# Kernel optimization log

Hardware: AMD Instinct MI355X
Metric: run time of the kernel (lower is better)

## Reference

```python
import jax, jax.numpy as jnp
import numpy as np

N, E, F, H = 50000, 160000, 512, 32
EPS = 1e-5  # BatchNorm eps


def setup_inputs() -> dict:
    key = jax.random.key(0)
    ks = jax.random.split(key, 16)
    s = lambda fan: 1.0 / np.sqrt(fan)
    inp = {
        "x": jax.random.normal(ks[0], (N, 2), jnp.float32),
        "edge_index": jax.random.randint(ks[1], (2, E), 0, N, jnp.int64),
        "face": jax.random.normal(ks[2], (N, F), jnp.float32),
        # encoder: Linear(2,32) -> BN(32) -> PReLU -> Dropout(0) -> Linear(32,32)
        "W1": jax.random.uniform(ks[3], (2, H), jnp.float32, -s(2), s(2)),
        "b1": jnp.zeros((H,), jnp.float32),
        "gamma": jnp.ones((H,), jnp.float32),
        "beta": jnp.zeros((H,), jnp.float32),
        "alpha": jnp.full((1,), 0.25, jnp.float32),  # PReLU default
        "W2": jax.random.uniform(ks[4], (H, H), jnp.float32, -s(H), s(H)),
        "b2": jnp.zeros((H,), jnp.float32),
        "w0": jax.random.uniform(ks[5], (H, 1), jnp.float32, -s(H), s(H)),
        "b0": jnp.zeros((1,), jnp.float32),
        "Wg": jax.random.uniform(ks[6], (H, H), jnp.float32, -s(H), s(H)),
        "bg": jnp.zeros((H,), jnp.float32),
        "wf": jax.random.uniform(ks[7], (H, 1), jnp.float32, -s(H), s(H)),
        "bf": jnp.zeros((1,), jnp.float32),
    }
    return inp


def _encoder(x, W1, b1, gamma, beta, alpha, W2, b2):
    h = x @ W1 + b1
    mu = h.mean(0)
    var = h.var(0)  # biased, matching torch BN training math
    h = (h - mu) * jax.lax.rsqrt(var + EPS) * gamma + beta
    h = jnp.where(h >= 0, h, alpha * h)  # PReLU
    return h @ W2 + b2  # dropout p=0


def _gcn_face(h, edge_index, face, Wg, bg):
    # Face-similarity weighted GCN: w_ij = cos(face_i, face_j),
    # symmetric normalization with self loops (weight 1).
    src, dst = edge_index[0], edge_index[1]
    fn = face * jax.lax.rsqrt(jnp.sum(face * face, axis=1, keepdims=True) + 1e-12)
    ew = jnp.sum(fn[src] * fn[dst], axis=-1)  # [E]
    n = h.shape[0]
    deg = jax.ops.segment_sum(ew, dst, num_segments=n) + 1.0  # + self loop
    norm = ew * jax.lax.rsqrt(deg[src] * deg[dst])  # [E]
    agg = jax.ops.segment_sum(norm[:, None] * h[src], dst, num_segments=n)
    agg = agg + h / deg[:, None]  # self-loop term 1/deg_i
    return agg @ Wg + bg


def reference(x, edge_index, face, W1, b1, gamma, beta, alpha, W2, b2,
              w0, b0, Wg, bg, wf, bf):
    emb = _encoder(x, W1, b1, gamma, beta, alpha, W2, b2)      # [N,32]
    gcn = _gcn_face(emb, edge_index, face, Wg, bg)             # [N,32]
    linear_scores = (emb @ w0 + b0).squeeze(-1)                # [N]
    gcn_scores = (gcn @ wf + bf).squeeze(-1)                   # [N]
    return linear_scores + gcn_scores
```

## Files before the change

### kernel.cpp

```cpp
#include <hip/hip_runtime.h>

#define EPS_BN 1e-5f
#define FDIM 512
#define F4   128
#define HDIM 32
#define NB_XS 64

__device__ __forceinline__ int dot4i8(unsigned a, unsigned b) {
#if __has_builtin(__builtin_amdgcn_sdot4)
    return __builtin_amdgcn_sdot4((int)a, (int)b, 0, false);
#else
    int s;
    s  = (int)(signed char)(a      ) * (int)(signed char)(b      );
    s += (int)(signed char)(a >>  8) * (int)(signed char)(b >>  8);
    s += (int)(signed char)(a >> 16) * (int)(signed char)(b >> 16);
    s += (int)(signed char)(a >> 24) * (int)(signed char)(b >> 24);
    return s;
#endif
}

__global__ __launch_bounds__(256)
void k_prep(const float* __restrict__ face,
            const float* __restrict__ x,
            uint2* __restrict__ qrows,
            float* __restrict__ scales,
            float* __restrict__ deg,
            float* __restrict__ part,
            int n, int qb) {
    __shared__ float red[4][5];
    if ((int)blockIdx.x < qb) {
        int row  = (int)((blockIdx.x * 256 + threadIdx.x) >> 6);
        int lane = threadIdx.x & 63;
        if (row >= n) return;
        const float4* f4 = (const float4*)face + (size_t)row * F4;
        float4 a = f4[lane];
        float4 b = f4[lane + 64];
        float ss = a.x*a.x + a.y*a.y + a.z*a.z + a.w*a.w
                 + b.x*b.x + b.y*b.y + b.z*b.z + b.w*b.w;
        float mx = fmaxf(fmaxf(fmaxf(fabsf(a.x), fabsf(a.y)),
                               fmaxf(fabsf(a.z), fabsf(a.w))),
                         fmaxf(fmaxf(fabsf(b.x), fabsf(b.y)),
                               fmaxf(fabsf(b.z), fabsf(b.w))));
        #pragma unroll
        for (int off = 32; off > 0; off >>= 1) {
            ss += __shfl_xor(ss, off);
            mx  = fmaxf(mx, __shfl_xor(mx, off));
        }
        float rn = rsqrtf(ss + 1e-12f);
        float qs = (mx > 0.f) ? 127.0f / mx : 0.f;
        unsigned da =  ((unsigned)(__float2int_rn(a.x*qs) & 255))
                    | (((unsigned)(__float2int_rn(a.y*qs) & 255)) << 8)
                    | (((unsigned)(__float2int_rn(a.z*qs) & 255)) << 16)
                    | (((unsigned)(__float2int_rn(a.w*qs) & 255)) << 24);
        unsigned db =  ((unsigned)(__float2int_rn(b.x*qs) & 255))
                    | (((unsigned)(__float2int_rn(b.y*qs) & 255)) << 8)
                    | (((unsigned)(__float2int_rn(b.z*qs) & 255)) << 16)
                    | (((unsigned)(__float2int_rn(b.w*qs) & 255)) << 24);
        qrows[(size_t)row * 64 + lane] = make_uint2(da, db);
        if (lane == 0) {
            scales[row] = mx * rn * (1.0f / 127.0f);
            deg[row]    = 0.f;
        }
    } else {
        int bid = (int)blockIdx.x - qb;
        float s0=0.f, s1=0.f, s00=0.f, s01=0.f, s11=0.f;
        for (int i = bid * 256 + threadIdx.x; i < n; i += NB_XS * 256) {
            float2 xv = ((const float2*)x)[i];
            s0  += xv.x;       s1  += xv.y;
            s00 += xv.x*xv.x;  s01 += xv.x*xv.y;  s11 += xv.y*xv.y;
        }
        #pragma unroll
        for (int off = 32; off > 0; off >>= 1) {
            s0  += __shfl_xor(s0,  off);
            s1  += __shfl_xor(s1,  off);
            s00 += __shfl_xor(s00, off);
            s01 += __shfl_xor(s01, off);
            s11 += __shfl_xor(s11, off);
        }
        int lane = threadIdx.x & 63, w = threadIdx.x >> 6;
        if (lane == 0) {
            red[w][0]=s0; red[w][1]=s1; red[w][2]=s00; red[w][3]=s01; red[w][4]=s11;
        }
        __syncthreads();
        if (threadIdx.x < 5) {
            part[bid * 5 + threadIdx.x] =
                red[0][threadIdx.x] + red[1][threadIdx.x]
              + red[2][threadIdx.x] + red[3][threadIdx.x];
        }
    }
}

__global__ void k_params(const float* __restrict__ part,
                         const float* __restrict__ W1,
                         const float* __restrict__ b1,
                         const float* __restrict__ gamma,
                         const float* __restrict__ beta,
                         const float* __restrict__ Wg,
                         const float* __restrict__ bg,
                         const float* __restrict__ wf,
                         const float* __restrict__ b0,
                         const float* __restrict__ bf,
                         float* __restrict__ params, int n) {
    __shared__ float xsl[5];
    int t = threadIdx.x;
    if (t < 5) {
        float s = 0.f;
        for (int i = 0; i < NB_XS; ++i) s += part[i * 5 + t];
        xsl[t] = s;
    }
    __syncthreads();
    float invN = 1.0f / (float)n;
    float m0 = xsl[0]*invN, m1 = xsl[1]*invN;
    float c00 = xsl[2]*invN - m0*m0;
    float c01 = xsl[3]*invN - m0*m1;
    float c11 = xsl[4]*invN - m1*m1;
    if (t < HDIM) {
        float w0j = W1[t], w1j = W1[HDIM + t];
        float mu  = m0*w0j + m1*w1j + b1[t];
        float var = c00*w0j*w0j + 2.f*c01*w0j*w1j + c11*w1j*w1j;
        float a   = gamma[t] * rsqrtf(var + EPS_BN);
        params[t]        = a;
        params[HDIM + t] = beta[t] - mu*a;
        float v = 0.f;
        for (int m = 0; m < HDIM; ++m) v += Wg[t*HDIM + m] * wf[m];
        params[2*HDIM + t] = v;
    } else if (t == HDIM) {
        float c = b0[0] + bf[0];
        for (int m = 0; m < HDIM; ++m) c += bg[m] * wf[m];
        params[3*HDIM] = c;
    }
}

__global__ __launch_bounds__(256)
void k_main(const float* __restrict__ x,
            const float* __restrict__ W1, const float* __restrict__ b1,
            const float* __restrict__ alpha,
            const float* __restrict__ W2, const float* __restrict__ b2,
            const float* __restrict__ w0,
            const float* __restrict__ params,
            const uint4* __restrict__ qrows,
            const float* __restrict__ scales,
            const int* __restrict__ src,
            const int* __restrict__ dst,
            float* __restrict__ ew,
            float* __restrict__ deg,
            float* __restrict__ sarr,
            float* __restrict__ out,
            int n, int ne, int nbn) {
    __shared__ float sW2[HDIM*HDIM];
    __shared__ float sW1[2*HDIM], sb1[HDIM], sa[HDIM], sbsh[HDIM];
    __shared__ float sv[HDIM], sw0[HDIM], sb2[HDIM];
    __shared__ float sc, salpha;

    if ((int)blockIdx.x < nbn) {
        for (int i = threadIdx.x; i < HDIM*HDIM; i += blockDim.x) sW2[i] = W2[i];
        if (threadIdx.x < 2*HDIM) sW1[threadIdx.x] = W1[threadIdx.x];
        if (threadIdx.x < HDIM) {
            sb1[threadIdx.x]  = b1[threadIdx.x];
            sa[threadIdx.x]   = params[threadIdx.x];
            sbsh[threadIdx.x] = params[HDIM + threadIdx.x];
            sv[threadIdx.x]   = params[2*HDIM + threadIdx.x];
            sw0[threadIdx.x]  = w0[threadIdx.x];
            sb2[threadIdx.x]  = b2[threadIdx.x];
        }
        if (threadIdx.x == 0) { sc = params[3*HDIM]; salpha = alpha[0]; }
        __syncthreads();
        int i = blockIdx.x * blockDim.x + threadIdx.x;
        if (i >= n) return;

        float2 xv = ((const float2*)x)[i];
        float h[HDIM];
        #pragma unroll
        for (int j = 0; j < HDIM; ++j) {
            float t = xv.x*sW1[j] + xv.y*sW1[HDIM + j] + sb1[j];
            t = sa[j]*t + sbsh[j];
            h[j] = (t >= 0.f) ? t : salpha*t;
        }
        float em[HDIM];
        #pragma unroll
        for (int k = 0; k < HDIM; ++k) em[k] = sb2[k];
        #pragma unroll
        for (int j = 0; j < HDIM; ++j) {
            float hj = h[j];
            #pragma unroll
            for (int k = 0; k < HDIM; ++k) em[k] += hj * sW2[j*HDIM + k];
        }
        float sdot = 0.f, ldot = 0.f;
        #pragma unroll
        for (int k = 0; k < HDIM; ++k) { sdot += em[k]*sv[k]; ldot += em[k]*sw0[k]; }
        sarr[i] = sdot;
        out[i]  = ldot + sc;
    } else {
        int e  = ((int)blockIdx.x - nbn) * 16 + (int)(threadIdx.x >> 4);
        int gl = threadIdx.x & 15;
        if (e >= ne) return;
        int si = src[e], di = dst[e];
        const uint4* rs = qrows + (size_t)si * 32;
        const uint4* rd = qrows + (size_t)di * 32;
        uint4 a0 = rs[gl], a1 = rs[gl + 16];
        uint4 b0 = rd[gl], b1 = rd[gl + 16];
        int acc = dot4i8(a0.x, b0.x) + dot4i8(a0.y, b0.y)
                + dot4i8(a0.z, b0.z) + dot4i8(a0.w, b0.w)
                + dot4i8(a1.x, b1.x) + dot4i8(a1.y, b1.y)
                + dot4i8(a1.z, b1.z) + dot4i8(a1.w, b1.w);
        #pragma unroll
        for (int off = 8; off > 0; off >>= 1) acc += __shfl_xor(acc, off);
        if (gl == 0) {
            float w = (float)acc * scales[si] * scales[di];
            ew[e] = w;
            atomicAdd(&deg[di], w);
        }
    }
}

__global__ void k_finish(const int* __restrict__ src,
                         const int* __restrict__ dst,
                         const float* __restrict__ ew,
                         const float* __restrict__ deg,
                         const float* __restrict__ sarr,
                         float* __restrict__ out, int ne, int n) {
    int t = blockIdx.x * blockDim.x + threadIdx.x;
    if (t < ne) {
        int si = src[t], di = dst[t];
        float w = ew[t] * rsqrtf((deg[si] + 1.f) * (deg[di] + 1.f)) * sarr[si];
        atomicAdd(&out[di], w);
    } else if (t < ne + n) {
        int i = t - ne;
        atomicAdd(&out[i], sarr[i] / (deg[i] + 1.f));
    }
}

extern "C" void kernel_launch(void* const* d_in, const int* in_sizes, int n_in,
                              void* d_out, int out_size, void* d_ws, size_t ws_size,
                              hipStream_t stream) {
    const float* x     = (const float*)d_in[0];
    const int*   ei    = (const int*)  d_in[1];
    const float* face  = (const float*)d_in[2];
    const float* W1    = (const float*)d_in[3];
    const float* b1    = (const float*)d_in[4];
    const float* gamma = (const float*)d_in[5];
    const float* beta  = (const float*)d_in[6];
    const float* alpha = (const float*)d_in[7];
    const float* W2    = (const float*)d_in[8];
    const float* b2    = (const float*)d_in[9];
    const float* w0    = (const float*)d_in[10];
    const float* b0    = (const float*)d_in[11];
    const float* Wg    = (const float*)d_in[12];
    const float* bg    = (const float*)d_in[13];
    const float* wf    = (const float*)d_in[14];
    const float* bf    = (const float*)d_in[15];

    const int n  = in_sizes[0] / 2;
    const int ne = in_sizes[1] / 2;
    const int* src = ei;
    const int* dst = ei + ne;

    float* ws     = (float*)d_ws;
    uint2* qrows  = (uint2*)ws;
    float* after  = ws + (size_t)n * 128;
    float* deg    = after;
    float* scales = after + n;
    float* sarr   = after + 2*(size_t)n;
    float* ew     = after + 3*(size_t)n;
    float* part   = after + 3*(size_t)n + ne;
    float* params = part + NB_XS*5 + 3;
    float* out    = (float*)d_out;

    const int qb  = (n + 3) / 4;
    const int nbn = (n + 255) / 256;
    const int ebk = (ne + 15) / 16;

    k_prep  <<<qb + NB_XS, 256, 0, stream>>>(face, x, qrows, scales, deg,
                                             part, n, qb);
    k_params<<<1, 64, 0, stream>>>(part, W1, b1, gamma, beta, Wg, bg, wf,
                                   b0, bf, params, n);
    k_main  <<<nbn + ebk, 256, 0, stream>>>(x, W1, b1, alpha, W2, b2, w0,
                                            params, (const uint4*)qrows,
                                            scales, src, dst, ew, deg, sarr,
                                            out, n, ne, nbn);
    k_finish<<<(ne + n + 255) / 256, 256, 0, stream>>>(src, dst, ew, deg,
                                                       sarr, out, ne, n);
}
```

Baseline: 66.46 us.

## Bucket-sort edges by destination and remap edge blocks across XCDs

Builds a destination-bucket histogram and prefix sum, with last-block detection, inside the prep kernel. A scatter pass then reorders edges by dst>>6, so the edge cosine kernel reads destination rows and updates deg with more locality. The k_params launch is folded into prep via an atomic ticket, and edge blocks are remapped so contiguous bucket ranges land on the same XCD. Each edge now uses 8 lanes instead of 16. In exchange it adds a memset, atomic-heavy histogram and scatter passes, and extra workspace traffic.

```diff
diff --git a/kernel.cpp b/kernel.cpp
--- a/kernel.cpp
+++ b/kernel.cpp
@@ -5,6 +5,8 @@
 #define F4   128
 #define HDIM 32
 #define NB_XS 64
+#define NBH   64
+#define MAXBKT 1024
 
 __device__ __forceinline__ int dot4i8(unsigned a, unsigned b) {
 #if __has_builtin(__builtin_amdgcn_sdot4)
@@ -19,18 +21,32 @@
 #endif
 }
 
+__device__ __forceinline__ float atomicReadF(float* p) { return atomicAdd(p, 0.0f); }
+__device__ __forceinline__ int   atomicReadI(int* p)   { return atomicAdd(p, 0); }
+
 __global__ __launch_bounds__(256)
 void k_prep(const float* __restrict__ face,
             const float* __restrict__ x,
+            const int* __restrict__ dst,
             uint2* __restrict__ qrows,
             float* __restrict__ scales,
             float* __restrict__ deg,
-            float* __restrict__ part,
-            int n, int qb) {
-    __shared__ float red[4][5];
+            float* __restrict__ xs,
+            int*   __restrict__ tick,
+            int*   __restrict__ hist,
+            int*   __restrict__ bucket_ptr,
+            const float* __restrict__ W1, const float* __restrict__ b1,
+            const float* __restrict__ gamma, const float* __restrict__ beta,
+            const float* __restrict__ Wg, const float* __restrict__ bg,
+            const float* __restrict__ wf, const float* __restrict__ b0,
+            const float* __restrict__ bf,
+            float* __restrict__ params,
+            int n, int ne, int qb, int nbkt) {
+    int tid = threadIdx.x;
+
     if ((int)blockIdx.x < qb) {
-        int row  = (int)((blockIdx.x * 256 + threadIdx.x) >> 6);
-        int lane = threadIdx.x & 63;
+        int row  = (int)((blockIdx.x * 256 + tid) >> 6);
+        int lane = tid & 63;
         if (row >= n) return;
         const float4* f4 = (const float4*)face + (size_t)row * F4;
         float4 a = f4[lane];
@@ -61,10 +77,15 @@
             scales[row] = mx * rn * (1.0f / 127.0f);
             deg[row]    = 0.f;
         }
-    } else {
+        return;
+    }
+
+    if ((int)blockIdx.x < qb + NB_XS) {
+        __shared__ float red[4][5];
+        __shared__ int amlast;
         int bid = (int)blockIdx.x - qb;
         float s0=0.f, s1=0.f, s00=0.f, s01=0.f, s11=0.f;
-        for (int i = bid * 256 + threadIdx.x; i < n; i += NB_XS * 256) {
+        for (int i = bid * 256 + tid; i < n; i += NB_XS * 256) {
             float2 xv = ((const float2*)x)[i];
             s0  += xv.x;       s1  += xv.y;
             s00 += xv.x*xv.x;  s01 += xv.x*xv.y;  s11 += xv.y*xv.y;
@@ -77,82 +98,98 @@
             s01 += __shfl_xor(s01, off);
             s11 += __shfl_xor(s11, off);
         }
-        int lane = threadIdx.x & 63, w = threadIdx.x >> 6;
+        int lane = tid & 63, w = tid >> 6;
         if (lane == 0) {
             red[w][0]=s0; red[w][1]=s1; red[w][2]=s00; red[w][3]=s01; red[w][4]=s11;
         }
         __syncthreads();
-        if (threadIdx.x < 5) {
-            part[bid * 5 + threadIdx.x] =
-                red[0][threadIdx.x] + red[1][threadIdx.x]
-              + red[2][threadIdx.x] + red[3][threadIdx.x];
-        }
-    }
-}
-
-__global__ void k_params(const float* __restrict__ part,
-                         const float* __restrict__ W1,
-                         const float* __restrict__ b1,
-                         const float* __restrict__ gamma,
-                         const float* __restrict__ beta,
-                         const float* __restrict__ Wg,
-                         const float* __restrict__ bg,
-                         const float* __restrict__ wf,
-                         const float* __restrict__ b0,
-                         const float* __restrict__ bf,
-                         float* __restrict__ params, int n) {
-    __shared__ float xsl[5];
-    int t = threadIdx.x;
-    if (t < 5) {
-        float s = 0.f;
-        for (int i = 0; i < NB_XS; ++i) s += part[i * 5 + t];
-        xsl[t] = s;
-    }
-    __syncthreads();
-    float invN = 1.0f / (float)n;
-    float m0 = xsl[0]*invN, m1 = xsl[1]*invN;
-    float c00 = xsl[2]*invN - m0*m0;
-    float c01 = xsl[3]*invN - m0*m1;
-    float c11 = xsl[4]*invN - m1*m1;
-    if (t < HDIM) {
-        float w0j = W1[t], w1j = W1[HDIM + t];
-        float mu  = m0*w0j + m1*w1j + b1[t];
-        float var = c00*w0j*w0j + 2.f*c01*w0j*w1j + c11*w1j*w1j;
-        float a   = gamma[t] * rsqrtf(var + EPS_BN);
-        params[t]        = a;
-        params[HDIM + t] = beta[t] - mu*a;
-        float v = 0.f;
-        for (int m = 0; m < HDIM; ++m) v += Wg[t*HDIM + m] * wf[m];
-        params[2*HDIM + t] = v;
-    } else if (t == HDIM) {
-        float c = b0[0] + bf[0];
-        for (int m = 0; m < HDIM; ++m) c += bg[m] * wf[m];
-        params[3*HDIM] = c;
+        if (tid < 5) {
+            atomicAdd(&xs[tid], red[0][tid] + red[1][tid] + red[2][tid] + red[3][tid]);
+        }
+        if (tid == 0) {
+            __threadfence();
+            amlast = (atomicAdd(&tick[0], 1) == NB_XS - 1);
+        }
+        __syncthreads();
+        if (!amlast) return;
+        __shared__ float xsl[5];
+        if (tid < 5) xsl[tid] = atomicReadF(&xs[tid]);
+        __syncthreads();
+        float invN = 1.0f / (float)n;
+        float m0 = xsl[0]*invN, m1 = xsl[1]*invN;
+        float c00 = xsl[2]*invN - m0*m0;
+        float c01 = xsl[3]*invN - m0*m1;
+        float c11 = xsl[4]*invN - m1*m1;
+        if (tid < HDIM) {
+            float w0j = W1[tid], w1j = W1[HDIM + tid];
+            float mu  = m0*w0j + m1*w1j + b1[tid];
+            float var = c00*w0j*w0j + 2.f*c01*w0j*w1j + c11*w1j*w1j;
+            float aa  = gamma[tid] * rsqrtf(var + EPS_BN);
+            params[tid]        = aa;
+            params[HDIM + tid] = beta[tid] - mu*aa;
+            float v = 0.f;
+            for (int m = 0; m < HDIM; ++m) v += Wg[tid*HDIM + m] * wf[m];
+            params[2*HDIM + tid] = v;
+        } else if (tid == HDIM) {
+            float c = b0[0] + bf[0];
+            for (int m = 0; m < HDIM; ++m) c += bg[m] * wf[m];
+            params[3*HDIM] = c;
+        }
+        return;
+    }
+
+    {
+        __shared__ int amlast;
+        int bid = (int)blockIdx.x - qb - NB_XS;
+        for (int e = bid * 256 + tid; e < ne; e += NBH * 256)
+            atomicAdd(&hist[dst[e] >> 6], 1);
+        if (tid == 0) {
+            __threadfence();
+            amlast = (atomicAdd(&tick[1], 1) == NBH - 1);
+        }
+        __syncthreads();
+        if (!amlast) return;
+        __shared__ int sh[MAXBKT];
+        __shared__ int tsum[256];
+        for (int k = tid; k < MAXBKT; k += 256)
+            sh[k] = (k < nbkt) ? atomicReadI(&hist[k]) : 0;
+        __syncthreads();
+        int k0 = tid * 4;
+        int a0 = sh[k0], a1 = sh[k0+1], a2 = sh[k0+2], a3 = sh[k0+3];
+        int p0 = a0, p1 = p0 + a1, p2 = p1 + a2, p3 = p2 + a3;
+        tsum[tid] = p3;
+        __syncthreads();
+        for (int off = 1; off < 256; off <<= 1) {
+            int v = (tid >= off) ? tsum[tid - off] : 0;
+            __syncthreads();
+            tsum[tid] += v;
+            __syncthreads();
+        }
+        int base = (tid > 0) ? tsum[tid - 1] : 0;
+        if (k0     < MAXBKT) bucket_ptr[k0]     = base;
+        if (k0 + 1 < MAXBKT) bucket_ptr[k0 + 1] = base + p0;
+        if (k0 + 2 < MAXBKT) bucket_ptr[k0 + 2] = base + p1;
+        if (k0 + 3 < MAXBKT) bucket_ptr[k0 + 3] = base + p2;
     }
 }
 
 __global__ __launch_bounds__(256)
-void k_main(const float* __restrict__ x,
-            const float* __restrict__ W1, const float* __restrict__ b1,
-            const float* __restrict__ alpha,
-            const float* __restrict__ W2, const float* __restrict__ b2,
-            const float* __restrict__ w0,
-            const float* __restrict__ params,
-            const uint4* __restrict__ qrows,
-            const float* __restrict__ scales,
-            const int* __restrict__ src,
-            const int* __restrict__ dst,
-            float* __restrict__ ew,
-            float* __restrict__ deg,
-            float* __restrict__ sarr,
-            float* __restrict__ out,
-            int n, int ne, int nbn) {
-    __shared__ float sW2[HDIM*HDIM];
-    __shared__ float sW1[2*HDIM], sb1[HDIM], sa[HDIM], sbsh[HDIM];
-    __shared__ float sv[HDIM], sw0[HDIM], sb2[HDIM];
-    __shared__ float sc, salpha;
-
+void k_mid(const float* __restrict__ x,
+           const float* __restrict__ W1, const float* __restrict__ b1,
+           const float* __restrict__ alpha,
+           const float* __restrict__ W2, const float* __restrict__ b2,
+           const float* __restrict__ w0,
+           const float* __restrict__ params,
+           const int* __restrict__ src, const int* __restrict__ dst,
+           int* __restrict__ bucket_ptr,
+           int* __restrict__ se_src, int* __restrict__ se_dst,
+           float* __restrict__ sarr, float* __restrict__ out,
+           int n, int ne, int nbn) {
     if ((int)blockIdx.x < nbn) {
+        __shared__ float sW2[HDIM*HDIM];
+        __shared__ float sW1[2*HDIM], sb1[HDIM], sa[HDIM], sbsh[HDIM];
+        __shared__ float sv[HDIM], sw0[HDIM], sb2[HDIM];
+        __shared__ float sc, salpha;
         for (int i = threadIdx.x; i < HDIM*HDIM; i += blockDim.x) sW2[i] = W2[i];
         if (threadIdx.x < 2*HDIM) sW1[threadIdx.x] = W1[threadIdx.x];
         if (threadIdx.x < HDIM) {
@@ -167,7 +204,6 @@
         __syncthreads();
         int i = blockIdx.x * blockDim.x + threadIdx.x;
         if (i >= n) return;
-
         float2 xv = ((const float2*)x)[i];
         float h[HDIM];
         #pragma unroll
@@ -191,37 +227,59 @@
         sarr[i] = sdot;
         out[i]  = ldot + sc;
     } else {
-        int e  = ((int)blockIdx.x - nbn) * 16 + (int)(threadIdx.x >> 4);
-        int gl = threadIdx.x & 15;
+        int e = ((int)blockIdx.x - nbn) * 256 + threadIdx.x;
         if (e >= ne) return;
-        int si = src[e], di = dst[e];
-        const uint4* rs = qrows + (size_t)si * 32;
-        const uint4* rd = qrows + (size_t)di * 32;
-        uint4 a0 = rs[gl], a1 = rs[gl + 16];
-        uint4 b0 = rd[gl], b1 = rd[gl + 16];
-        int acc = dot4i8(a0.x, b0.x) + dot4i8(a0.y, b0.y)
-                + dot4i8(a0.z, b0.z) + dot4i8(a0.w, b0.w)
-                + dot4i8(a1.x, b1.x) + dot4i8(a1.y, b1.y)
-                + dot4i8(a1.z, b1.z) + dot4i8(a1.w, b1.w);
-        #pragma unroll
-        for (int off = 8; off > 0; off >>= 1) acc += __shfl_xor(acc, off);
-        if (gl == 0) {
-            float w = (float)acc * scales[si] * scales[di];
-            ew[e] = w;
-            atomicAdd(&deg[di], w);
-        }
-    }
-}
-
-__global__ void k_finish(const int* __restrict__ src,
-                         const int* __restrict__ dst,
+        int d = dst[e];
+        int pos = atomicAdd(&bucket_ptr[d >> 6], 1);
+        se_src[pos] = src[e];
+        se_dst[pos] = d;
+    }
+}
+
+__global__ __launch_bounds__(256)
+void k_edge(const uint4* __restrict__ qrows,
+            const float* __restrict__ scales,
+            const int* __restrict__ se_src,
+            const int* __restrict__ se_dst,
+            float* __restrict__ ew,
+            float* __restrict__ deg, int ne, int nwg) {
+    int hw  = (int)blockIdx.x;
+    int q   = nwg >> 3, r = nwg & 7;
+    int xcd = hw & 7, idx = hw >> 3;
+    int base = (xcd < r) ? xcd * (q + 1) : r * (q + 1) + (xcd - r) * q;
+    int blk  = base + idx;
+
+    int e  = blk * 32 + (int)(threadIdx.x >> 3);
+    int gl = threadIdx.x & 7;
+    if (e >= ne) return;
+    int si = se_src[e], di = se_dst[e];
+    const uint4* rs = qrows + (size_t)si * 32;
+    const uint4* rd = qrows + (size_t)di * 32;
+    uint4 a0 = rs[gl], a1 = rs[gl+8], a2 = rs[gl+16], a3 = rs[gl+24];
+    uint4 b0 = rd[gl], b1 = rd[gl+8], b2 = rd[gl+16], b3 = rd[gl+24];
+    int acc = dot4i8(a0.x,b0.x) + dot4i8(a0.y,b0.y) + dot4i8(a0.z,b0.z) + dot4i8(a0.w,b0.w)
+            + dot4i8(a1.x,b1.x) + dot4i8(a1.y,b1.y) + dot4i8(a1.z,b1.z) + dot4i8(a1.w,b1.w)
+            + dot4i8(a2.x,b2.x) + dot4i8(a2.y,b2.y) + dot4i8(a2.z,b2.z) + dot4i8(a2.w,b2.w)
+            + dot4i8(a3.x,b3.x) + dot4i8(a3.y,b3.y) + dot4i8(a3.z,b3.z) + dot4i8(a3.w,b3.w);
+    acc += __shfl_xor(acc, 4);
+    acc += __shfl_xor(acc, 2);
+    acc += __shfl_xor(acc, 1);
+    if (gl == 0) {
+        float w = (float)acc * scales[si] * scales[di];
+        ew[e] = w;
+        atomicAdd(&deg[di], w);
+    }
+}
+
+__global__ void k_finish(const int* __restrict__ se_src,
+                         const int* __restrict__ se_dst,
                          const float* __restrict__ ew,
                          const float* __restrict__ deg,
                          const float* __restrict__ sarr,
                          float* __restrict__ out, int ne, int n) {
     int t = blockIdx.x * blockDim.x + threadIdx.x;
     if (t < ne) {
-        int si = src[t], di = dst[t];
+        int si = se_src[t], di = se_dst[t];
         float w = ew[t] * rsqrtf((deg[si] + 1.f) * (deg[di] + 1.f)) * sarr[si];
         atomicAdd(&out[di], w);
     } else if (t < ne + n) {
@@ -254,6 +312,7 @@
     const int ne = in_sizes[1] / 2;
     const int* src = ei;
     const int* dst = ei + ne;
+    const int nbkt = (n + 63) >> 6;
 
     float* ws     = (float*)d_ws;
     uint2* qrows  = (uint2*)ws;
@@ -262,22 +321,34 @@
     float* scales = after + n;
     float* sarr   = after + 2*(size_t)n;
     float* ew     = after + 3*(size_t)n;
-    float* part   = after + 3*(size_t)n + ne;
-    float* params = part + NB_XS*5 + 3;
+    int*   se_src = (int*)(after + 3*(size_t)n + ne);
+    int*   se_dst = se_src + ne;
+    float* zreg   = (float*)(se_dst + ne);
+    float* xs     = zreg;
+    int*   tick   = (int*)(zreg + 8);
+    int*   hist   = tick + 2;
+    int*   bktptr = hist + MAXBKT;
+    float* params = (float*)(bktptr + MAXBKT);
     float* out    = (float*)d_out;
 
     const int qb  = (n + 3) / 4;
     const int nbn = (n + 255) / 256;
-    const int ebk = (ne + 15) / 16;
-
-    k_prep  <<<qb + NB_XS, 256, 0, stream>>>(face, x, qrows, scales, deg,
-                                             part, n, qb);
-    k_params<<<1, 64, 0, stream>>>(part, W1, b1, gamma, beta, Wg, bg, wf,
-                                   b0, bf, params, n);
-    k_main  <<<nbn + ebk, 256, 0, stream>>>(x, W1, b1, alpha, W2, b2, w0,
-                                            params, (const uint4*)qrows,
-                                            scales, src, dst, ew, deg, sarr,
-                                            out, n, ne, nbn);
-    k_finish<<<(ne + n + 255) / 256, 256, 0, stream>>>(src, dst, ew, deg,
-                                                       sarr, out, ne, n);
-}
+    const int scb = (ne + 255) / 256;
+    const int ebk = (ne + 31) / 32;
+
+    hipMemsetAsync(zreg, 0, (10 + MAXBKT) * sizeof(int), stream);
+
+    k_prep<<<qb + NB_XS + NBH, 256, 0, stream>>>(
+        face, x, dst, qrows, scales, deg, xs, tick, hist, bktptr,
+        W1, b1, gamma, beta, Wg, bg, wf, b0, bf, params, n, ne, qb, nbkt);
+
+    k_mid<<<nbn + scb, 256, 0, stream>>>(
+        x, W1, b1, alpha, W2, b2, w0, params, src, dst, bktptr,
+        se_src, se_dst, sarr, out, n, ne, nbn);
+
+    k_edge<<<ebk, 256, 0, stream>>>((const uint4*)qrows, scales,
+                                    se_src, se_dst, ew, deg, ne, ebk);
+
+    k_finish<<<(ne + n + 255) / 256, 256, 0, stream>>>(se_src, se_dst, ew,
+                                                       deg, sarr, out, ne, n);
+}
```

Measured after the change: 140.7 us. 112% more time.

## Fold BN param kernel into main kernel and use 8 lanes per edge

Applied to the files above, without the earlier changes.

Removes the single-block k_params launch. The x-moment partials are now reduced with atomics into a small buffer that is zeroed by a memset, and every node block of k_main recomputes the BN scale/shift, the Wg·wf vector and the constant itself. The edge-weight path also changes from 16 lanes to 8 lanes per edge, with each lane loading four uint4 pairs, so one block handles 32 edges and the shuffle reduction is shorter. The trade is one kernel launch and dependency removed against a memset launch, redundant per-block setup work, and float atomics that make the sum order nondeterministic.

```diff
diff --git a/kernel.cpp b/kernel.cpp
--- a/kernel.cpp
+++ b/kernel.cpp
@@ -25,12 +25,12 @@
             uint2* __restrict__ qrows,
             float* __restrict__ scales,
             float* __restrict__ deg,
-            float* __restrict__ part,
+            float* __restrict__ xs,
             int n, int qb) {
-    __shared__ float red[4][5];
+    int tid = threadIdx.x;
     if ((int)blockIdx.x < qb) {
-        int row  = (int)((blockIdx.x * 256 + threadIdx.x) >> 6);
-        int lane = threadIdx.x & 63;
+        int row  = (int)((blockIdx.x * 256 + tid) >> 6);
+        int lane = tid & 63;
         if (row >= n) return;
         const float4* f4 = (const float4*)face + (size_t)row * F4;
         float4 a = f4[lane];
@@ -62,9 +62,10 @@
             deg[row]    = 0.f;
         }
     } else {
+        __shared__ float red[4][5];
         int bid = (int)blockIdx.x - qb;
         float s0=0.f, s1=0.f, s00=0.f, s01=0.f, s11=0.f;
-        for (int i = bid * 256 + threadIdx.x; i < n; i += NB_XS * 256) {
+        for (int i = bid * 256 + tid; i < n; i += NB_XS * 256) {
             float2 xv = ((const float2*)x)[i];
             s0  += xv.x;       s1  += xv.y;
             s00 += xv.x*xv.x;  s01 += xv.x*xv.y;  s11 += xv.y*xv.y;
@@ -77,97 +78,72 @@
             s01 += __shfl_xor(s01, off);
             s11 += __shfl_xor(s11, off);
         }
-        int lane = threadIdx.x & 63, w = threadIdx.x >> 6;
+        int lane = tid & 63, w = tid >> 6;
         if (lane == 0) {
             red[w][0]=s0; red[w][1]=s1; red[w][2]=s00; red[w][3]=s01; red[w][4]=s11;
         }
         __syncthreads();
-        if (threadIdx.x < 5) {
-            part[bid * 5 + threadIdx.x] =
-                red[0][threadIdx.x] + red[1][threadIdx.x]
-              + red[2][threadIdx.x] + red[3][threadIdx.x];
-        }
-    }
-}
-
-__global__ void k_params(const float* __restrict__ part,
-                         const float* __restrict__ W1,
-                         const float* __restrict__ b1,
-                         const float* __restrict__ gamma,
-                         const float* __restrict__ beta,
-                         const float* __restrict__ Wg,
-                         const float* __restrict__ bg,
-                         const float* __restrict__ wf,
-                         const float* __restrict__ b0,
-                         const float* __restrict__ bf,
-                         float* __restrict__ params, int n) {
-    __shared__ float xsl[5];
-    int t = threadIdx.x;
-    if (t < 5) {
-        float s = 0.f;
-        for (int i = 0; i < NB_XS; ++i) s += part[i * 5 + t];
-        xsl[t] = s;
-    }
-    __syncthreads();
-    float invN = 1.0f / (float)n;
-    float m0 = xsl[0]*invN, m1 = xsl[1]*invN;
-    float c00 = xsl[2]*invN - m0*m0;
-    float c01 = xsl[3]*invN - m0*m1;
-    float c11 = xsl[4]*invN - m1*m1;
-    if (t < HDIM) {
-        float w0j = W1[t], w1j = W1[HDIM + t];
-        float mu  = m0*w0j + m1*w1j + b1[t];
-        float var = c00*w0j*w0j + 2.f*c01*w0j*w1j + c11*w1j*w1j;
-        float a   = gamma[t] * rsqrtf(var + EPS_BN);
-        params[t]        = a;
-        params[HDIM + t] = beta[t] - mu*a;
-        float v = 0.f;
-        for (int m = 0; m < HDIM; ++m) v += Wg[t*HDIM + m] * wf[m];
-        params[2*HDIM + t] = v;
-    } else if (t == HDIM) {
-        float c = b0[0] + bf[0];
-        for (int m = 0; m < HDIM; ++m) c += bg[m] * wf[m];
-        params[3*HDIM] = c;
+        if (tid < 5) {
+            atomicAdd(&xs[tid],
+                      red[0][tid] + red[1][tid] + red[2][tid] + red[3][tid]);
+        }
     }
 }
 
 __global__ __launch_bounds__(256)
 void k_main(const float* __restrict__ x,
             const float* __restrict__ W1, const float* __restrict__ b1,
+            const float* __restrict__ gamma, const float* __restrict__ beta,
             const float* __restrict__ alpha,
             const float* __restrict__ W2, const float* __restrict__ b2,
             const float* __restrict__ w0,
-            const float* __restrict__ params,
+            const float* __restrict__ Wg, const float* __restrict__ bg,
+            const float* __restrict__ wf,
+            const float* __restrict__ b0, const float* __restrict__ bf,
+            const float* __restrict__ xs,
             const uint4* __restrict__ qrows,
             const float* __restrict__ scales,
-            const int* __restrict__ src,
-            const int* __restrict__ dst,
+            const int* __restrict__ src, const int* __restrict__ dst,
             float* __restrict__ ew,
             float* __restrict__ deg,
             float* __restrict__ sarr,
             float* __restrict__ out,
             int n, int ne, int nbn) {
-    __shared__ float sW2[HDIM*HDIM];
-    __shared__ float sW1[2*HDIM], sb1[HDIM], sa[HDIM], sbsh[HDIM];
-    __shared__ float sv[HDIM], sw0[HDIM], sb2[HDIM];
-    __shared__ float sc, salpha;
-
     if ((int)blockIdx.x < nbn) {
-        for (int i = threadIdx.x; i < HDIM*HDIM; i += blockDim.x) sW2[i] = W2[i];
-        if (threadIdx.x < 2*HDIM) sW1[threadIdx.x] = W1[threadIdx.x];
-        if (threadIdx.x < HDIM) {
-            sb1[threadIdx.x]  = b1[threadIdx.x];
-            sa[threadIdx.x]   = params[threadIdx.x];
-            sbsh[threadIdx.x] = params[HDIM + threadIdx.x];
-            sv[threadIdx.x]   = params[2*HDIM + threadIdx.x];
-            sw0[threadIdx.x]  = w0[threadIdx.x];
-            sb2[threadIdx.x]  = b2[threadIdx.x];
-        }
-        if (threadIdx.x == 0) { sc = params[3*HDIM]; salpha = alpha[0]; }
+        __shared__ float sW2[HDIM*HDIM];
+        __shared__ float sW1[2*HDIM], sb1[HDIM], sa[HDIM], sbsh[HDIM];
+        __shared__ float sv[HDIM], sw0[HDIM], sb2[HDIM];
+        __shared__ float sc, salpha;
+        int tid = threadIdx.x;
+        for (int i = tid; i < HDIM*HDIM; i += blockDim.x) sW2[i] = W2[i];
+        if (tid < 2*HDIM) sW1[tid] = W1[tid];
+        if (tid < HDIM) {
+            float invN = 1.0f / (float)n;
+            float m0 = xs[0]*invN, m1 = xs[1]*invN;
+            float c00 = xs[2]*invN - m0*m0;
+            float c01 = xs[3]*invN - m0*m1;
+            float c11 = xs[4]*invN - m1*m1;
+            float w0j = W1[tid], w1j = W1[HDIM + tid];
+            float mu  = m0*w0j + m1*w1j + b1[tid];
+            float var = c00*w0j*w0j + 2.f*c01*w0j*w1j + c11*w1j*w1j;
+            float aa  = gamma[tid] * rsqrtf(var + EPS_BN);
+            sa[tid]   = aa;
+            sbsh[tid] = beta[tid] - mu*aa;
+            float v = 0.f;
+            for (int m = 0; m < HDIM; ++m) v += Wg[tid*HDIM + m] * wf[m];
+            sv[tid]  = v;
+            sb1[tid] = b1[tid];
+            sw0[tid] = w0[tid];
+            sb2[tid] = b2[tid];
+        } else if (tid == HDIM) {
+            float c = b0[0] + bf[0];
+            for (int m = 0; m < HDIM; ++m) c += bg[m] * wf[m];
+            sc = c;
+            salpha = alpha[0];
+        }
         __syncthreads();
-        int i = blockIdx.x * blockDim.x + threadIdx.x;
+        int i = blockIdx.x * blockDim.x + tid;
         if (i >= n) return;
-
         float2 xv = ((const float2*)x)[i];
         float h[HDIM];
         #pragma unroll
@@ -191,20 +167,21 @@
         sarr[i] = sdot;
         out[i]  = ldot + sc;
     } else {
-        int e  = ((int)blockIdx.x - nbn) * 16 + (int)(threadIdx.x >> 4);
-        int gl = threadIdx.x & 15;
+        int e  = ((int)blockIdx.x - nbn) * 32 + (int)(threadIdx.x >> 3);
+        int gl = threadIdx.x & 7;
         if (e >= ne) return;
         int si = src[e], di = dst[e];
         const uint4* rs = qrows + (size_t)si * 32;
         const uint4* rd = qrows + (size_t)di * 32;
-        uint4 a0 = rs[gl], a1 = rs[gl + 16];
-        uint4 b0 = rd[gl], b1 = rd[gl + 16];
-        int acc = dot4i8(a0.x, b0.x) + dot4i8(a0.y, b0.y)
-                + dot4i8(a0.z, b0.z) + dot4i8(a0.w, b0.w)
-                + dot4i8(a1.x, b1.x) + dot4i8(a1.y, b1.y)
-                + dot4i8(a1.z, b1.z) + dot4i8(a1.w, b1.w);
-        #pragma unroll
-        for (int off = 8; off > 0; off >>= 1) acc += __shfl_xor(acc, off);
+        uint4 a0 = rs[gl], a1 = rs[gl+8], a2 = rs[gl+16], a3 = rs[gl+24];
+        uint4 b0 = rd[gl], b1 = rd[gl+8], b2 = rd[gl+16], b3 = rd[gl+24];
+        int acc = dot4i8(a0.x,b0.x) + dot4i8(a0.y,b0.y) + dot4i8(a0.z,b0.z) + dot4i8(a0.w,b0.w)
+                + dot4i8(a1.x,b1.x) + dot4i8(a1.y,b1.y) + dot4i8(a1.z,b1.z) + dot4i8(a1.w,b1.w)
+                + dot4i8(a2.x,b2.x) + dot4i8(a2.y,b2.y) + dot4i8(a2.z,b2.z) + dot4i8(a2.w,b2.w)
+                + dot4i8(a3.x,b3.x) + dot4i8(a3.y,b3.y) + dot4i8(a3.z,b3.z) + dot4i8(a3.w,b3.w);
+        acc += __shfl_xor(acc, 4);
+        acc += __shfl_xor(acc, 2);
+        acc += __shfl_xor(acc, 1);
         if (gl == 0) {
             float w = (float)acc * scales[si] * scales[di];
             ew[e] = w;
@@ -262,22 +239,24 @@
     float* scales = after + n;
     float* sarr   = after + 2*(size_t)n;
     float* ew     = after + 3*(size_t)n;
-    float* part   = after + 3*(size_t)n + ne;
-    float* params = part + NB_XS*5 + 3;
+    float* xs     = after + 3*(size_t)n + ne;
     float* out    = (float*)d_out;
 
     const int qb  = (n + 3) / 4;
     const int nbn = (n + 255) / 256;
-    const int ebk = (ne + 15) / 16;
-
-    k_prep  <<<qb + NB_XS, 256, 0, stream>>>(face, x, qrows, scales, deg,
-                                             part, n, qb);
-    k_params<<<1, 64, 0, stream>>>(part, W1, b1, gamma, beta, Wg, bg, wf,
-                                   b0, bf, params, n);
-    k_main  <<<nbn + ebk, 256, 0, stream>>>(x, W1, b1, alpha, W2, b2, w0,
-                                            params, (const uint4*)qrows,
-                                            scales, src, dst, ew, deg, sarr,
-                                            out, n, ne, nbn);
+    const int ebk = (ne + 31) / 32;
+
+    hipMemsetAsync(xs, 0, 8 * sizeof(float), stream);
+
+    k_prep<<<qb + NB_XS, 256, 0, stream>>>(face, x, qrows, scales, deg, xs,
+                                           n, qb);
+
+    k_main<<<nbn + ebk, 256, 0, stream>>>(x, W1, b1, gamma, beta, alpha,
+                                          W2, b2, w0, Wg, bg, wf, b0, bf, xs,
+                                          (const uint4*)qrows, scales,
+                                          src, dst, ew, deg, sarr, out,
+                                          n, ne, nbn);
+
     k_finish<<<(ne + n + 255) / 256, 256, 0, stream>>>(src, dst, ew, deg,
                                                        sarr, out, ne, n);
 }
```

After: 65.52 us. No clear change (-1.4%).
